# Kernel tuning notes

Measured on AMD Instinct MI355X. Metric: run time of the kernel, lower is better.

The kernel has to match this reference:

```python
import jax, jax.numpy as jnp
import numpy as np

N = 100000
E = 1600000
D = 128
LAYERS = 2


def setup_inputs() -> dict:
    key = jax.random.key(0)
    k1, k2, k3, k4, k5, k6 = jax.random.split(key, 6)
    features = jax.random.normal(k1, (N, D), dtype=jnp.float32)
    edge_row = jax.random.randint(k2, (E,), 0, N)
    edge_col = jax.random.randint(k3, (E,), 0, N)
    edge_val = jax.random.uniform(k4, (E,), dtype=jnp.float32)
    # new_features[index] = out_features with out_features having N rows =>
    # index is a permutation covering all N nodes
    index = jax.random.permutation(k5, N)
    a_in = jax.random.normal(k6, (3,), dtype=jnp.float32)
    return {"features": features, "edge_row": edge_row, "edge_col": edge_col,
            "edge_val": edge_val, "index": index, "a_in": a_in}


def reference(features, edge_row, edge_col, edge_val, index, a_in):
    n, d = features.shape
    # --- normalize_adj: D^{-1/2} A D^{-1/2} (Mat is constant across layers) ---
    rowsum = jax.ops.segment_sum(edge_val, edge_row, num_segments=n)  # [N]
    d_inv_sqrt = jnp.where(rowsum > 0, rowsum ** -0.5, 0.0)
    vals = d_inv_sqrt[edge_row] * edge_val * d_inv_sqrt[edge_col]      # [E]

    # softmax over first Layers+1 entries of a_in
    a = jax.nn.softmax(a_in[:LAYERS + 1])

    # nodes covered by index keep the SpMM result; others keep old features
    covered = jnp.zeros((n,), dtype=bool).at[index].set(True)

    result = a[0] * features
    h = features
    for j in range(LAYERS):
        # SpMM: out[r] = sum_e vals[e] * h[col[e]] for row[e] == r
        out = jax.ops.segment_sum(vals[:, None] * h[edge_col], edge_row,
                                  num_segments=n)                      # [N, D]
        scattered = jnp.zeros_like(h).at[index].set(out)
        h = jnp.where(covered[:, None], scattered, h)
        result = result + a[j + 1] * h
    return result
```

## Files before the change

kernel.cpp:

```cpp
#include <hip/hip_runtime.h>

#define WPB    4
#define SCAN_B 1024
#define P1B    256
#define BKT_SH 8

__device__ __forceinline__ unsigned bf16rne(float x) {
  unsigned u = __float_as_uint(x);
  return (u + 0x7fffu + ((u >> 16) & 1u)) >> 16;
}
__device__ __forceinline__ float bf_lo(unsigned g) { return __uint_as_float(g << 16); }
__device__ __forceinline__ float bf_hi(unsigned g) { return __uint_as_float(g & 0xffff0000u); }

__global__ void prep_k(const float2* __restrict__ f, unsigned* __restrict__ hb, int nw,
                       const float* __restrict__ a_in, float* __restrict__ a_buf,
                       const int* __restrict__ index, int* __restrict__ covered,
                       int* __restrict__ row_start, int E, int N) {
  int i = blockIdx.x * 256 + threadIdx.x;
  if (i < nw) {
    float2 v = f[i];
    hb[i] = bf16rne(v.x) | (bf16rne(v.y) << 16);
  }
  if (i < N) covered[index[i]] = 1;
  if (i == 0) {
    row_start[N] = E;
    float x0 = a_in[0], x1 = a_in[1], x2 = a_in[2];
    float m = fmaxf(x0, fmaxf(x1, x2));
    float e0 = expf(x0 - m), e1 = expf(x1 - m), e2 = expf(x2 - m);
    float s = e0 + e1 + e2;
    a_buf[0] = e0 / s; a_buf[1] = e1 / s; a_buf[2] = e2 / s;
  }
}

__global__ void p1_k(const int* __restrict__ row, int* __restrict__ bhist,
                     int E, int C, int NB) {
  extern __shared__ int h[];
  for (int k = threadIdx.x; k < NB; k += 256) h[k] = 0;
  __syncthreads();
  int s = blockIdx.x * C, e = min(E, s + C);
  for (int i = s + threadIdx.x; i < e; i += 256)
    atomicAdd(&h[row[i] >> BKT_SH], 1);
  __syncthreads();
  for (int k = threadIdx.x; k < NB; k += 256)
    bhist[(size_t)k * P1B + blockIdx.x] = h[k];
}

__global__ void scanA_k(const int* __restrict__ cnt, int* __restrict__ incl,
                        int* __restrict__ bsum, int n) {
  __shared__ int tmp[SCAN_B];
  int tid = threadIdx.x;
  int g = blockIdx.x * SCAN_B + tid;
  tmp[tid] = (g < n) ? cnt[g] : 0;
  __syncthreads();
  for (int off = 1; off < SCAN_B; off <<= 1) {
    int t = (tid >= off) ? tmp[tid - off] : 0;
    __syncthreads();
    tmp[tid] += t;
    __syncthreads();
  }
  if (g < n) incl[g] = tmp[tid];
  if (tid == SCAN_B - 1) bsum[blockIdx.x] = tmp[tid];
}

__global__ void scanB_k(int* __restrict__ bsum, int nb) {
  __shared__ int tmp[128];
  int tid = threadIdx.x;
  tmp[tid] = (tid < nb) ? bsum[tid] : 0;
  __syncthreads();
  for (int off = 1; off < 128; off <<= 1) {
    int t = (tid >= off) ? tmp[tid - off] : 0;
    __syncthreads();
    tmp[tid] += t;
    __syncthreads();
  }
  if (tid < nb) bsum[tid] = tmp[tid];
}

__global__ void scanC_k(int* __restrict__ boffs, const int* __restrict__ bhist,
                        const int* __restrict__ bsum, int n) {
  int g = blockIdx.x * SCAN_B + threadIdx.x;
  if (g >= n) return;
  int off = (blockIdx.x > 0) ? bsum[blockIdx.x - 1] : 0;
  boffs[g] = boffs[g] + off - bhist[g];
}

__global__ void p2_k(const int* __restrict__ row, const int* __restrict__ col,
                     const float* __restrict__ val, const int* __restrict__ boffs,
                     int2* __restrict__ bedge, int E, int C, int NB) {
  extern __shared__ int cur[];
  for (int k = threadIdx.x; k < NB; k += 256)
    cur[k] = boffs[(size_t)k * P1B + blockIdx.x];
  __syncthreads();
  int s = blockIdx.x * C, e = min(E, s + C);
  for (int i = s + threadIdx.x; i < e; i += 256) {
    int r = row[i];
    int p = atomicAdd(&cur[r >> BKT_SH], 1);
    bedge[p] = make_int2(((r & 255) << 24) | col[i], __float_as_int(val[i]));
  }
}

__global__ void p3_k(const int2* __restrict__ bedge, const int* __restrict__ boffs,
                     int* __restrict__ row_start, float* __restrict__ dis,
                     int2* __restrict__ pairs, int E, int N, int NB) {
  __shared__ int rcnt[256];
  __shared__ float rsum[256];
  __shared__ int rbase[256];
  __shared__ int tmp[256];
  int kb = blockIdx.x, t = threadIdx.x;
  int base = boffs[(size_t)kb * P1B];
  int end  = (kb + 1 < NB) ? boffs[(size_t)(kb + 1) * P1B] : E;
  rcnt[t] = 0; rsum[t] = 0.f;
  __syncthreads();
  for (int i = base + t; i < end; i += 256) {
    int2 p = bedge[i];
    int rlo = ((unsigned)p.x) >> 24;
    atomicAdd(&rcnt[rlo], 1);
    atomicAdd(&rsum[rlo], __int_as_float(p.y));
  }
  __syncthreads();
  int v = rcnt[t];
  tmp[t] = v;
  __syncthreads();
  for (int off = 1; off < 256; off <<= 1) {
    int u = (t >= off) ? tmp[t - off] : 0;
    __syncthreads();
    tmp[t] += u;
    __syncthreads();
  }
  rbase[t] = tmp[t] - v;
  int r = (kb << BKT_SH) + t;
  if (r < N) {
    row_start[r] = base + rbase[t];
    float s = rsum[t];
    dis[r] = (s > 0.0f) ? rsqrtf(s) : 0.0f;
  }
  __syncthreads();
  rcnt[t] = rbase[t];
  __syncthreads();
  for (int i = base + t; i < end; i += 256) {
    int2 p = bedge[i];
    int rlo = ((unsigned)p.x) >> 24;
    int pos = base + atomicAdd(&rcnt[rlo], 1);
    pairs[pos] = make_int2(p.x & 0xFFFFFF, p.y);
  }
}

__global__ void scale_k(int2* __restrict__ pairs, const float* __restrict__ dis, int E) {
  int i = blockIdx.x * 256 + threadIdx.x;
  if (i < E) {
    int2 p = pairs[i];
    p.y = __float_as_int(__int_as_float(p.y) * dis[p.x]);
    pairs[i] = p;
  }
}

__device__ __forceinline__ void acc8(float v, uint4 g, float* a) {
  a[0] = fmaf(v, bf_lo(g.x), a[0]); a[1] = fmaf(v, bf_hi(g.x), a[1]);
  a[2] = fmaf(v, bf_lo(g.y), a[2]); a[3] = fmaf(v, bf_hi(g.y), a[3]);
  a[4] = fmaf(v, bf_lo(g.z), a[4]); a[5] = fmaf(v, bf_hi(g.z), a[5]);
  a[6] = fmaf(v, bf_lo(g.w), a[6]); a[7] = fmaf(v, bf_hi(g.w), a[7]);
}

__device__ __forceinline__ void spmm_body(const int* __restrict__ row_start,
                                          const int2* __restrict__ pairs,
                                          const uint4* __restrict__ h4,
                                          int wave, int lane, float* a) {
  int q = lane >> 4, ql = lane & 15;
  int beg = row_start[wave], end = row_start[wave + 1];
  for (int base = beg; base < end; base += 64) {
    int2 p = make_int2(0, 0);
    if (base + lane < end) p = pairs[base + lane];
    int pc = p.x; float pv = __int_as_float(p.y);
    int m = end - base; if (m > 64) m = 64;
    for (int j = 0; j < m; j += 16) {
      int   c0 = __shfl(pc, j + q),      c1 = __shfl(pc, j + 4 + q);
      int   c2 = __shfl(pc, j + 8 + q),  c3 = __shfl(pc, j + 12 + q);
      float v0 = __shfl(pv, j + q),      v1 = __shfl(pv, j + 4 + q);
      float v2 = __shfl(pv, j + 8 + q),  v3 = __shfl(pv, j + 12 + q);
      uint4 g0 = h4[(size_t)c0 * 16 + ql];
      uint4 g1 = h4[(size_t)c1 * 16 + ql];
      uint4 g2 = h4[(size_t)c2 * 16 + ql];
      uint4 g3 = h4[(size_t)c3 * 16 + ql];
      acc8(v0, g0, a); acc8(v1, g1, a);
      acc8(v2, g2, a); acc8(v3, g3, a);
    }
  }
#pragma unroll
  for (int i = 0; i < 8; ++i) a[i] += __shfl_xor(a[i], 16);
#pragma unroll
  for (int i = 0; i < 8; ++i) a[i] += __shfl_xor(a[i], 32);
}

__global__ void spmm1_k(const int* __restrict__ row_start, const int2* __restrict__ pairs,
                        const float* __restrict__ dis, const uint4* __restrict__ hB4,
                        const int* __restrict__ index, uint4* __restrict__ hA4, int n) {
  int wave = blockIdx.x * WPB + (threadIdx.x >> 6);
  if (wave >= n) return;
  int lane = threadIdx.x & 63;
  float a[8] = {0.f, 0.f, 0.f, 0.f, 0.f, 0.f, 0.f, 0.f};
  spmm_body(row_start, pairs, hB4, wave, lane, a);
  if ((lane >> 4) == 0) {
    float dr = dis[wave];
    uint4 pk;
    pk.x = bf16rne(a[0] * dr) | (bf16rne(a[1] * dr) << 16);
    pk.y = bf16rne(a[2] * dr) | (bf16rne(a[3] * dr) << 16);
    pk.z = bf16rne(a[4] * dr) | (bf16rne(a[5] * dr) << 16);
    pk.w = bf16rne(a[6] * dr) | (bf16rne(a[7] * dr) << 16);
    hA4[(size_t)index[wave] * 16 + (lane & 15)] = pk;
  }
}

__global__ void spmm2_k(const int* __restrict__ row_start, const int2* __restrict__ pairs,
                        const float* __restrict__ dis, const uint4* __restrict__ hA4,
                        const uint4* __restrict__ hB4, const int* __restrict__ index,
                        float4* __restrict__ out4, const float* __restrict__ ac, int n) {
  int wave = blockIdx.x * WPB + (threadIdx.x >> 6);
  if (wave >= n) return;
  int lane = threadIdx.x & 63;
  float a[8] = {0.f, 0.f, 0.f, 0.f, 0.f, 0.f, 0.f, 0.f};
  spmm_body(row_start, pairs, hA4, wave, lane, a);
  if ((lane >> 4) == 0) {
    int ql = lane & 15;
    float dr = dis[wave];
    size_t ro = (size_t)index[wave] * 16 + ql;
    uint4 ga = hA4[ro];
    uint4 gb = hB4[ro];
    float c0 = ac[0], c1 = ac[1], c2 = ac[2];
    float4 w0, w1;
    w0.x = fmaf(c2, a[0] * dr, fmaf(c1, bf_lo(ga.x), c0 * bf_lo(gb.x)));
    w0.y = fmaf(c2, a[1] * dr, fmaf(c1, bf_hi(ga.x), c0 * bf_hi(gb.x)));
    w0.z = fmaf(c2, a[2] * dr, fmaf(c1, bf_lo(ga.y), c0 * bf_lo(gb.y)));
    w0.w = fmaf(c2, a[3] * dr, fmaf(c1, bf_hi(ga.y), c0 * bf_hi(gb.y)));
    w1.x = fmaf(c2, a[4] * dr, fmaf(c1, bf_lo(ga.z), c0 * bf_lo(gb.z)));
    w1.y = fmaf(c2, a[5] * dr, fmaf(c1, bf_hi(ga.z), c0 * bf_hi(gb.z)));
    w1.z = fmaf(c2, a[6] * dr, fmaf(c1, bf_lo(ga.w), c0 * bf_lo(gb.w)));
    w1.w = fmaf(c2, a[7] * dr, fmaf(c1, bf_hi(ga.w), c0 * bf_hi(gb.w)));
    out4[(size_t)index[wave] * 32 + 2 * ql]     = w0;
    out4[(size_t)index[wave] * 32 + 2 * ql + 1] = w1;
  }
}

__global__ void fixup1_k(const int* __restrict__ covered, const uint4* __restrict__ hB4,
                         uint4* __restrict__ hA4, int n) {
  int v = blockIdx.x * 256 + threadIdx.x;
  if (v >= n || covered[v]) return;
  for (int d = 0; d < 16; ++d) hA4[(size_t)v * 16 + d] = hB4[(size_t)v * 16 + d];
}

__global__ void fixup2_k(const int* __restrict__ covered, const float2* __restrict__ feat,
                         float2* __restrict__ out, const float* __restrict__ a, int n) {
  int v = blockIdx.x * 256 + threadIdx.x;
  if (v >= n || covered[v]) return;
  float s = a[0] + a[1] + a[2];
  for (int d = 0; d < 64; ++d) {
    float2 f = feat[(size_t)v * 64 + d];
    out[(size_t)v * 64 + d] = make_float2(s * f.x, s * f.y);
  }
}

extern "C" void kernel_launch(void* const* d_in, const int* in_sizes, int n_in,
                              void* d_out, int out_size, void* d_ws, size_t ws_size,
                              hipStream_t stream) {
  const float* features = (const float*)d_in[0];
  const int*   edge_row = (const int*)d_in[1];
  const int*   edge_col = (const int*)d_in[2];
  const float* edge_val = (const float*)d_in[3];
  const int*   index    = (const int*)d_in[4];
  const float* a_in     = (const float*)d_in[5];

  const int E = in_sizes[1];
  const int N = in_sizes[4];
  const int NB = (N + 255) >> BKT_SH;
  const int NBH = NB * P1B;
  const int C = (E + P1B - 1) / P1B;

  float* out = (float*)d_out;

  char* ws = (char*)d_ws;
  size_t off = 0;
  auto carve = [&](size_t bytes) -> char* {
    char* p = ws + off;
    off = (off + bytes + 255) & ~(size_t)255;
    return p;
  };
  float* a_buf     = (float*)carve(16 * sizeof(float));
  float* dis       = (float*)carve((size_t)N * 4);
  int*   covered   = (int*)carve((size_t)N * 4);
  int*   row_start = (int*)carve((size_t)(N + 1) * 4);
  int*   bsum      = (int*)carve(256 * 4);
  int2*  pairs     = (int2*)carve((size_t)E * 8);
  unsigned* hB     = (unsigned*)carve((size_t)N * 64 * 4);
  size_t ov_bytes = (size_t)NBH * 4 * 2 + (size_t)E * 8 + 1024;
  size_t hA_bytes = (size_t)N * 64 * 4;
  char* ovl = carve(ov_bytes > hA_bytes ? ov_bytes : hA_bytes);
  int*  bhist = (int*)ovl;
  int*  boffs = (int*)(ovl + (((size_t)NBH * 4 + 255) & ~(size_t)255));
  int2* bedge = (int2*)(ovl + 2 * (((size_t)NBH * 4 + 255) & ~(size_t)255));
  unsigned* hA = (unsigned*)ovl;
  (void)ws_size; (void)n_in; (void)out_size;

  const int nbE = (E + 255) / 256;
  const int nbW = (N * 64 + 255) / 256;
  const int nbScan = (NBH + SCAN_B - 1) / SCAN_B;
  const int nbN = (N + 255) / 256;
  const size_t ldsB = (size_t)NB * 4;

  hipMemsetAsync(covered, 0, (size_t)N * 4, stream);
  prep_k<<<nbW, 256, 0, stream>>>((const float2*)features, hB, N * 64,
                                  a_in, a_buf, index, covered, row_start, E, N);
  p1_k<<<P1B, 256, ldsB, stream>>>(edge_row, bhist, E, C, NB);
  scanA_k<<<nbScan, SCAN_B, 0, stream>>>(bhist, boffs, bsum, NBH);
  scanB_k<<<1, 128, 0, stream>>>(bsum, nbScan);
  scanC_k<<<nbScan, SCAN_B, 0, stream>>>(boffs, bhist, bsum, NBH);
  p2_k<<<P1B, 256, ldsB, stream>>>(edge_row, edge_col, edge_val, boffs, bedge, E, C, NB);
  p3_k<<<NB, 256, 0, stream>>>(bedge, boffs, row_start, dis, pairs, E, N, NB);
  scale_k<<<nbE, 256, 0, stream>>>(pairs, dis, E);

  const int nbSpmm = (N + WPB - 1) / WPB;
  spmm1_k<<<nbSpmm, WPB * 64, 0, stream>>>(row_start, pairs, dis, (const uint4*)hB,
                                           index, (uint4*)hA, N);
  fixup1_k<<<nbN, 256, 0, stream>>>(covered, (const uint4*)hB, (uint4*)hA, N);
  spmm2_k<<<nbSpmm, WPB * 64, 0, stream>>>(row_start, pairs, dis, (const uint4*)hA,
                                           (const uint4*)hB, index, (float4*)out,
                                           a_buf, N);
  fixup2_k<<<nbN, 256, 0, stream>>>(covered, (const float2*)features,
                                    (float2*)out, a_buf, N);
}
```

Measured before the change: 219.0 us.

## Fuse prep with histogram and scan stages, fold column scaling into SpMM

Merges the bf16 conversion kernel with the row-bucket histogram, merges the two scan fixup kernels into one, and removes the separate edge-scaling pass by multiplying by dis[col] inside the SpMM gather. It also adds nontemporal loads and stores for streamed data and switches to 32-bit address arithmetic in the gather. The aim is fewer launches and one less full pass over the edge array, at the cost of an extra dis lookup per edge in each SpMM, and redundant per-block recomputation of the small scan.

```diff
diff --git a/kernel.cpp b/kernel.cpp
--- a/kernel.cpp
+++ b/kernel.cpp
@@ -5,6 +5,10 @@
 #define P1B    256
 #define BKT_SH 8
 
+typedef unsigned u32x4 __attribute__((ext_vector_type(4)));
+typedef float    f32x4 __attribute__((ext_vector_type(4)));
+typedef float    f32x2 __attribute__((ext_vector_type(2)));
+
 __device__ __forceinline__ unsigned bf16rne(float x) {
   unsigned u = __float_as_uint(x);
   return (u + 0x7fffu + ((u >> 16) & 1u)) >> 16;
@@ -12,13 +16,20 @@
 __device__ __forceinline__ float bf_lo(unsigned g) { return __uint_as_float(g << 16); }
 __device__ __forceinline__ float bf_hi(unsigned g) { return __uint_as_float(g & 0xffff0000u); }
 
-__global__ void prep_k(const float2* __restrict__ f, unsigned* __restrict__ hb, int nw,
-                       const float* __restrict__ a_in, float* __restrict__ a_buf,
-                       const int* __restrict__ index, int* __restrict__ covered,
-                       int* __restrict__ row_start, int E, int N) {
+__global__ void prep_p1_k(const f32x2* __restrict__ f, unsigned* __restrict__ hb, int nw,
+                          const float* __restrict__ a_in, float* __restrict__ a_buf,
+                          const int* __restrict__ index, int* __restrict__ covered,
+                          int* __restrict__ row_start, const int* __restrict__ erow,
+                          int* __restrict__ bhist, int E, int N, int C, int NB) {
+  extern __shared__ int h[];
+  const bool dop1 = (blockIdx.x < P1B);
+  if (dop1) {
+    for (int k = threadIdx.x; k < NB; k += 256) h[k] = 0;
+    __syncthreads();
+  }
   int i = blockIdx.x * 256 + threadIdx.x;
   if (i < nw) {
-    float2 v = f[i];
+    f32x2 v = __builtin_nontemporal_load(f + i);
     hb[i] = bf16rne(v.x) | (bf16rne(v.y) << 16);
   }
   if (i < N) covered[index[i]] = 1;
@@ -30,19 +41,14 @@
     float s = e0 + e1 + e2;
     a_buf[0] = e0 / s; a_buf[1] = e1 / s; a_buf[2] = e2 / s;
   }
-}
-
-__global__ void p1_k(const int* __restrict__ row, int* __restrict__ bhist,
-                     int E, int C, int NB) {
-  extern __shared__ int h[];
-  for (int k = threadIdx.x; k < NB; k += 256) h[k] = 0;
-  __syncthreads();
-  int s = blockIdx.x * C, e = min(E, s + C);
-  for (int i = s + threadIdx.x; i < e; i += 256)
-    atomicAdd(&h[row[i] >> BKT_SH], 1);
-  __syncthreads();
-  for (int k = threadIdx.x; k < NB; k += 256)
-    bhist[(size_t)k * P1B + blockIdx.x] = h[k];
+  if (dop1) {
+    int s = blockIdx.x * C, e = min(E, s + C);
+    for (int j = s + threadIdx.x; j < e; j += 256)
+      atomicAdd(&h[erow[j] >> BKT_SH], 1);
+    __syncthreads();
+    for (int k = threadIdx.x; k < NB; k += 256)
+      bhist[(size_t)k * P1B + blockIdx.x] = h[k];
+  }
 }
 
 __global__ void scanA_k(const int* __restrict__ cnt, int* __restrict__ incl,
@@ -62,26 +68,23 @@
   if (tid == SCAN_B - 1) bsum[blockIdx.x] = tmp[tid];
 }
 
-__global__ void scanB_k(int* __restrict__ bsum, int nb) {
-  __shared__ int tmp[128];
+__global__ void scanBC_k(int* __restrict__ boffs, const int* __restrict__ bhist,
+                         const int* __restrict__ bsum, int nb, int n) {
+  __shared__ int bs[128];
   int tid = threadIdx.x;
-  tmp[tid] = (tid < nb) ? bsum[tid] : 0;
+  if (tid < 128) bs[tid] = (tid < nb) ? bsum[tid] : 0;
   __syncthreads();
   for (int off = 1; off < 128; off <<= 1) {
-    int t = (tid >= off) ? tmp[tid - off] : 0;
-    __syncthreads();
-    tmp[tid] += t;
-    __syncthreads();
-  }
-  if (tid < nb) bsum[tid] = tmp[tid];
-}
-
-__global__ void scanC_k(int* __restrict__ boffs, const int* __restrict__ bhist,
-                        const int* __restrict__ bsum, int n) {
-  int g = blockIdx.x * SCAN_B + threadIdx.x;
-  if (g >= n) return;
-  int off = (blockIdx.x > 0) ? bsum[blockIdx.x - 1] : 0;
-  boffs[g] = boffs[g] + off - bhist[g];
+    int t = (tid >= off && tid < 128) ? bs[tid - off] : 0;
+    __syncthreads();
+    if (tid < 128) bs[tid] += t;
+    __syncthreads();
+  }
+  int g = blockIdx.x * SCAN_B + tid;
+  if (g < n) {
+    int off2 = (blockIdx.x > 0) ? bs[blockIdx.x - 1] : 0;
+    boffs[g] = boffs[g] + off2 - bhist[g];
+  }
 }
 
 __global__ void p2_k(const int* __restrict__ row, const int* __restrict__ col,
@@ -145,16 +148,7 @@
   }
 }
 
-__global__ void scale_k(int2* __restrict__ pairs, const float* __restrict__ dis, int E) {
-  int i = blockIdx.x * 256 + threadIdx.x;
-  if (i < E) {
-    int2 p = pairs[i];
-    p.y = __float_as_int(__int_as_float(p.y) * dis[p.x]);
-    pairs[i] = p;
-  }
-}
-
-__device__ __forceinline__ void acc8(float v, uint4 g, float* a) {
+__device__ __forceinline__ void acc8(float v, u32x4 g, float* a) {
   a[0] = fmaf(v, bf_lo(g.x), a[0]); a[1] = fmaf(v, bf_hi(g.x), a[1]);
   a[2] = fmaf(v, bf_lo(g.y), a[2]); a[3] = fmaf(v, bf_hi(g.y), a[3]);
   a[4] = fmaf(v, bf_lo(g.z), a[4]); a[5] = fmaf(v, bf_hi(g.z), a[5]);
@@ -163,24 +157,28 @@
 
 __device__ __forceinline__ void spmm_body(const int* __restrict__ row_start,
                                           const int2* __restrict__ pairs,
-                                          const uint4* __restrict__ h4,
+                                          const float* __restrict__ dis,
+                                          const char* __restrict__ hb,
                                           int wave, int lane, float* a) {
-  int q = lane >> 4, ql = lane & 15;
+  int q = lane >> 4;
+  unsigned qoff = (unsigned)(lane & 15) << 4;
   int beg = row_start[wave], end = row_start[wave + 1];
   for (int base = beg; base < end; base += 64) {
-    int2 p = make_int2(0, 0);
-    if (base + lane < end) p = pairs[base + lane];
-    int pc = p.x; float pv = __int_as_float(p.y);
+    unsigned long long pl = 0;
+    if (base + lane < end)
+      pl = __builtin_nontemporal_load((const unsigned long long*)(pairs + base + lane));
+    int pc = (int)(pl & 0xffffffffu);
+    float pv = __uint_as_float((unsigned)(pl >> 32)) * dis[pc];
     int m = end - base; if (m > 64) m = 64;
     for (int j = 0; j < m; j += 16) {
       int   c0 = __shfl(pc, j + q),      c1 = __shfl(pc, j + 4 + q);
       int   c2 = __shfl(pc, j + 8 + q),  c3 = __shfl(pc, j + 12 + q);
       float v0 = __shfl(pv, j + q),      v1 = __shfl(pv, j + 4 + q);
       float v2 = __shfl(pv, j + 8 + q),  v3 = __shfl(pv, j + 12 + q);
-      uint4 g0 = h4[(size_t)c0 * 16 + ql];
-      uint4 g1 = h4[(size_t)c1 * 16 + ql];
-      uint4 g2 = h4[(size_t)c2 * 16 + ql];
-      uint4 g3 = h4[(size_t)c3 * 16 + ql];
+      u32x4 g0 = *(const u32x4*)(hb + (((unsigned)c0 << 8) | qoff));
+      u32x4 g1 = *(const u32x4*)(hb + (((unsigned)c1 << 8) | qoff));
+      u32x4 g2 = *(const u32x4*)(hb + (((unsigned)c2 << 8) | qoff));
+      u32x4 g3 = *(const u32x4*)(hb + (((unsigned)c3 << 8) | qoff));
       acc8(v0, g0, a); acc8(v1, g1, a);
       acc8(v2, g2, a); acc8(v3, g3, a);
     }
@@ -192,41 +190,41 @@
 }
 
 __global__ void spmm1_k(const int* __restrict__ row_start, const int2* __restrict__ pairs,
-                        const float* __restrict__ dis, const uint4* __restrict__ hB4,
-                        const int* __restrict__ index, uint4* __restrict__ hA4, int n) {
+                        const float* __restrict__ dis, const unsigned* __restrict__ hB,
+                        const int* __restrict__ index, u32x4* __restrict__ hA4, int n) {
   int wave = blockIdx.x * WPB + (threadIdx.x >> 6);
   if (wave >= n) return;
   int lane = threadIdx.x & 63;
   float a[8] = {0.f, 0.f, 0.f, 0.f, 0.f, 0.f, 0.f, 0.f};
-  spmm_body(row_start, pairs, hB4, wave, lane, a);
+  spmm_body(row_start, pairs, dis, (const char*)hB, wave, lane, a);
   if ((lane >> 4) == 0) {
     float dr = dis[wave];
-    uint4 pk;
+    u32x4 pk;
     pk.x = bf16rne(a[0] * dr) | (bf16rne(a[1] * dr) << 16);
     pk.y = bf16rne(a[2] * dr) | (bf16rne(a[3] * dr) << 16);
     pk.z = bf16rne(a[4] * dr) | (bf16rne(a[5] * dr) << 16);
     pk.w = bf16rne(a[6] * dr) | (bf16rne(a[7] * dr) << 16);
-    hA4[(size_t)index[wave] * 16 + (lane & 15)] = pk;
+    hA4[(unsigned)index[wave] * 16u + (unsigned)(lane & 15)] = pk;
   }
 }
 
 __global__ void spmm2_k(const int* __restrict__ row_start, const int2* __restrict__ pairs,
-                        const float* __restrict__ dis, const uint4* __restrict__ hA4,
-                        const uint4* __restrict__ hB4, const int* __restrict__ index,
-                        float4* __restrict__ out4, const float* __restrict__ ac, int n) {
+                        const float* __restrict__ dis, const u32x4* __restrict__ hA4,
+                        const u32x4* __restrict__ hB4, const int* __restrict__ index,
+                        f32x4* __restrict__ out4, const float* __restrict__ ac, int n) {
   int wave = blockIdx.x * WPB + (threadIdx.x >> 6);
   if (wave >= n) return;
   int lane = threadIdx.x & 63;
   float a[8] = {0.f, 0.f, 0.f, 0.f, 0.f, 0.f, 0.f, 0.f};
-  spmm_body(row_start, pairs, hA4, wave, lane, a);
+  spmm_body(row_start, pairs, dis, (const char*)hA4, wave, lane, a);
   if ((lane >> 4) == 0) {
-    int ql = lane & 15;
+    unsigned ql = lane & 15;
     float dr = dis[wave];
-    size_t ro = (size_t)index[wave] * 16 + ql;
-    uint4 ga = hA4[ro];
-    uint4 gb = hB4[ro];
+    unsigned ro = (unsigned)index[wave] * 16u + ql;
+    u32x4 ga = hA4[ro];
+    u32x4 gb = __builtin_nontemporal_load(hB4 + ro);
     float c0 = ac[0], c1 = ac[1], c2 = ac[2];
-    float4 w0, w1;
+    f32x4 w0, w1;
     w0.x = fmaf(c2, a[0] * dr, fmaf(c1, bf_lo(ga.x), c0 * bf_lo(gb.x)));
     w0.y = fmaf(c2, a[1] * dr, fmaf(c1, bf_hi(ga.x), c0 * bf_hi(gb.x)));
     w0.z = fmaf(c2, a[2] * dr, fmaf(c1, bf_lo(ga.y), c0 * bf_lo(gb.y)));
@@ -235,13 +233,14 @@
     w1.y = fmaf(c2, a[5] * dr, fmaf(c1, bf_hi(ga.z), c0 * bf_hi(gb.z)));
     w1.z = fmaf(c2, a[6] * dr, fmaf(c1, bf_lo(ga.w), c0 * bf_lo(gb.w)));
     w1.w = fmaf(c2, a[7] * dr, fmaf(c1, bf_hi(ga.w), c0 * bf_hi(gb.w)));
-    out4[(size_t)index[wave] * 32 + 2 * ql]     = w0;
-    out4[(size_t)index[wave] * 32 + 2 * ql + 1] = w1;
-  }
-}
-
-__global__ void fixup1_k(const int* __restrict__ covered, const uint4* __restrict__ hB4,
-                         uint4* __restrict__ hA4, int n) {
+    unsigned ob = (unsigned)index[wave] * 32u + 2u * ql;
+    __builtin_nontemporal_store(w0, out4 + ob);
+    __builtin_nontemporal_store(w1, out4 + ob + 1);
+  }
+}
+
+__global__ void fixup1_k(const int* __restrict__ covered, const u32x4* __restrict__ hB4,
+                         u32x4* __restrict__ hA4, int n) {
   int v = blockIdx.x * 256 + threadIdx.x;
   if (v >= n || covered[v]) return;
   for (int d = 0; d < 16; ++d) hA4[(size_t)v * 16 + d] = hB4[(size_t)v * 16 + d];
@@ -299,29 +298,26 @@
   unsigned* hA = (unsigned*)ovl;
   (void)ws_size; (void)n_in; (void)out_size;
 
-  const int nbE = (E + 255) / 256;
   const int nbW = (N * 64 + 255) / 256;
   const int nbScan = (NBH + SCAN_B - 1) / SCAN_B;
   const int nbN = (N + 255) / 256;
   const size_t ldsB = (size_t)NB * 4;
 
   hipMemsetAsync(covered, 0, (size_t)N * 4, stream);
-  prep_k<<<nbW, 256, 0, stream>>>((const float2*)features, hB, N * 64,
-                                  a_in, a_buf, index, covered, row_start, E, N);
-  p1_k<<<P1B, 256, ldsB, stream>>>(edge_row, bhist, E, C, NB);
+  prep_p1_k<<<nbW, 256, ldsB, stream>>>((const f32x2*)features, hB, N * 64,
+                                        a_in, a_buf, index, covered, row_start,
+                                        edge_row, bhist, E, N, C, NB);
   scanA_k<<<nbScan, SCAN_B, 0, stream>>>(bhist, boffs, bsum, NBH);
-  scanB_k<<<1, 128, 0, stream>>>(bsum, nbScan);
-  scanC_k<<<nbScan, SCAN_B, 0, stream>>>(boffs, bhist, bsum, NBH);
+  scanBC_k<<<nbScan, SCAN_B, 0, stream>>>(boffs, bhist, bsum, nbScan, NBH);
   p2_k<<<P1B, 256, ldsB, stream>>>(edge_row, edge_col, edge_val, boffs, bedge, E, C, NB);
   p3_k<<<NB, 256, 0, stream>>>(bedge, boffs, row_start, dis, pairs, E, N, NB);
-  scale_k<<<nbE, 256, 0, stream>>>(pairs, dis, E);
 
   const int nbSpmm = (N + WPB - 1) / WPB;
-  spmm1_k<<<nbSpmm, WPB * 64, 0, stream>>>(row_start, pairs, dis, (const uint4*)hB,
-                                           index, (uint4*)hA, N);
-  fixup1_k<<<nbN, 256, 0, stream>>>(covered, (const uint4*)hB, (uint4*)hA, N);
-  spmm2_k<<<nbSpmm, WPB * 64, 0, stream>>>(row_start, pairs, dis, (const uint4*)hA,
-                                           (const uint4*)hB, index, (float4*)out,
+  spmm1_k<<<nbSpmm, WPB * 64, 0, stream>>>(row_start, pairs, dis, hB, index,
+                                           (u32x4*)hA, N);
+  fixup1_k<<<nbN, 256, 0, stream>>>(covered, (const u32x4*)hB, (u32x4*)hA, N);
+  spmm2_k<<<nbSpmm, WPB * 64, 0, stream>>>(row_start, pairs, dis, (const u32x4*)hA,
+                                           (const u32x4*)hB, index, (f32x4*)out,
                                            a_buf, N);
   fixup2_k<<<nbN, 256, 0, stream>>>(covered, (const float2*)features,
                                     (float2*)out, a_buf, N);
```

After: 212.8 us. 1.03x faster.
